# Performance work log

Hardware: AMD Instinct MI355X
Metric: run time of the kernel (lower is better)

Reference implementation:

```python
import jax, jax.numpy as jnp
import numpy as np

N = 200_000   # nodes in batched graph
E = 400_000   # edges
D = 128       # embed_dim
L = 5         # num_layer
G = 1000      # number of graphs in batch
ATOM_V = 119  # atom vocab (OGB)
BOND_V = 5    # bond vocab (OGB)
OUT = 128     # output_dim
EPS = 1e-5


def setup_inputs() -> dict:
    key = jax.random.key(0)
    ks = jax.random.split(key, 16)
    inp = {
        "nfeat": jax.random.randint(ks[0], (N,), 0, ATOM_V),
        "efeat": jax.random.randint(ks[1], (E,), 0, BOND_V),
        "src": jax.random.randint(ks[2], (E,), 0, N),
        "dst": jax.random.randint(ks[3], (E,), 0, N),
        "node2graph": jnp.sort(jax.random.randint(ks[4], (N,), 0, G)),
        # learned parameters
        "atom_emb": jax.random.normal(ks[5], (ATOM_V, D), jnp.float32) * 0.02,
        "edge_emb": jax.random.normal(ks[6], (L, BOND_V, D), jnp.float32) * 0.02,
        "W": jax.random.normal(ks[7], (L, D, D), jnp.float32) * 0.02,
        "b": jnp.zeros((L, D), jnp.float32),
        "gamma": jnp.ones((L, D), jnp.float32),
        "beta": jnp.zeros((L, D), jnp.float32),
        "W1": jax.random.normal(ks[8], (D, D), jnp.float32) * 0.02,
        "b1": jnp.zeros((D,), jnp.float32),
        "W2": jax.random.normal(ks[9], (D, OUT), jnp.float32) * 0.02,
        "b2": jnp.zeros((OUT,), jnp.float32),
    }
    return inp


def reference(nfeat, efeat, src, dst, node2graph,
              atom_emb, edge_emb, W, b, gamma, beta, W1, b1, W2, b2):
    h = atom_emb[nfeat]                                  # [N, D]
    # in-degree + 1 (GCNConvLayer degree norm)
    deg = jax.ops.segment_sum(jnp.ones((E,), h.dtype), dst, num_segments=N) + 1.0
    for l in range(L):
        e = edge_emb[l][efeat]                           # [E, D] edge encoder
        m = h[src] + e                                   # u_add_e
        neigh = jax.ops.segment_sum(m, dst, num_segments=N)  # fn.sum -> 'neigh'
        h = ((h + neigh) / deg[:, None]) @ W[l] + b[l]   # project_node_feat
        # batch norm over nodes (training-mode batch stats), affine
        mu = jnp.mean(h, axis=0)
        var = jnp.var(h, axis=0)
        h = (h - mu) * jax.lax.rsqrt(var + EPS) * gamma[l] + beta[l]
        h = jax.nn.relu(h)                               # activation; dropout=eval
    # global mean pooling per graph
    cnt = jax.ops.segment_sum(jnp.ones((N,), h.dtype), node2graph, num_segments=G)
    g = jax.ops.segment_sum(h, node2graph, num_segments=G) / jnp.maximum(cnt, 1.0)[:, None]
    # predict MLP (dropout in eval mode = identity)
    out = jax.nn.relu(g @ W1 + b1) @ W2 + b2             # [G, OUT]
    return out
```

## Files before the change

kernel.cpp:

```cpp
#include <hip/hip_runtime.h>
#include <hip/hip_bf16.h>
#include <cstddef>

#define NN 200000
#define NE 400000
#define DD 128
#define NL 5
#define NG 1000
#define BOND_V 5
#define BM 32
#define NBLK (NN / BM)
#define MAXD 16
#define PCH 200
#define NB_SCAN 200
#define CH 1000
#define SB 125
#define EPS 1e-5f
#define XS 136

typedef __bf16 bf16x8 __attribute__((ext_vector_type(8)));
typedef float floatx4 __attribute__((ext_vector_type(4)));

__device__ __forceinline__ unsigned short f2bf(float f) {
    unsigned int u = __float_as_uint(f);
    u = (u + 0x7fffu + ((u >> 16) & 1u)) >> 16;
    return (unsigned short)u;
}
__device__ __forceinline__ float bf2f(unsigned short s) {
    return __uint_as_float(((unsigned int)s) << 16);
}
__device__ __forceinline__ float4 bf4_to_f4(uint2 v) {
    float4 o;
    o.x = __uint_as_float(v.x << 16);
    o.y = __uint_as_float(v.x & 0xffff0000u);
    o.z = __uint_as_float(v.y << 16);
    o.w = __uint_as_float(v.y & 0xffff0000u);
    return o;
}
__device__ __forceinline__ float4 actv4(float4 h, float4 sc, float4 sh) {
    float4 o;
    o.x = fmaxf(0.f, h.x * sc.x + sh.x);
    o.y = fmaxf(0.f, h.y * sc.y + sh.y);
    o.z = fmaxf(0.f, h.z * sc.z + sh.z);
    o.w = fmaxf(0.f, h.w * sc.w + sh.w);
    return o;
}

__global__ void k_setup1(const int* __restrict__ dst, int* __restrict__ cnt,
                         const int* __restrict__ n2g, float* __restrict__ gcnt,
                         const float* __restrict__ W, unsigned short* __restrict__ Wht,
                         unsigned short* __restrict__ Wlt) {
    int e = blockIdx.x * blockDim.x + threadIdx.x;
    if (e < NE) atomicAdd(&cnt[dst[e]], 1);
    if (e < NN) atomicAdd(&gcnt[n2g[e]], 1.0f);
    if (e < NL * DD * DD) {
        int l = e / (DD * DD), rem = e % (DD * DD);
        int k = rem / DD, n = rem % DD;
        float v = W[e];
        unsigned short hb = f2bf(v);
        unsigned short lb = f2bf(v - bf2f(hb));
        size_t o = (size_t)l * DD * DD + (size_t)n * DD + k;
        Wht[o] = hb; Wlt[o] = lb;
    }
}

__global__ void k_scan1(const int* __restrict__ cnt, int* __restrict__ bsum) {
    __shared__ int sh[256];
    int b = blockIdx.x, t = threadIdx.x;
    int s = 0;
    if (t < CH / 4) {
        int base = b * CH + t * 4;
        s = cnt[base] + cnt[base + 1] + cnt[base + 2] + cnt[base + 3];
    }
    sh[t] = s;
    __syncthreads();
    if (t == 0) {
        int tot = 0;
        for (int i = 0; i < CH / 4; i++) tot += sh[i];
        bsum[b] = tot;
    }
}

__global__ void k_scan2(const int* __restrict__ bsum, int* __restrict__ bpre,
                        int* __restrict__ off) {
    if (threadIdx.x == 0) {
        int run = 0;
        for (int i = 0; i < NB_SCAN; i++) { bpre[i] = run; run += bsum[i]; }
        off[NN] = NE;
    }
}

__global__ void k_scan3(const int* __restrict__ cnt, const int* __restrict__ bpre,
                        int* __restrict__ off, int* __restrict__ cur,
                        float* __restrict__ rdeg) {
    __shared__ int sh[256];
    int b = blockIdx.x, t = threadIdx.x;
    int base = b * CH + t * 4;
    int c0 = 0, c1 = 0, c2 = 0, c3 = 0, s = 0;
    if (t < CH / 4) {
        c0 = cnt[base]; c1 = cnt[base + 1]; c2 = cnt[base + 2]; c3 = cnt[base + 3];
        s = c0 + c1 + c2 + c3;
    }
    sh[t] = s;
    __syncthreads();
    if (t == 0) {
        int run = bpre[b];
        for (int i = 0; i < CH / 4; i++) { int v = sh[i]; sh[i] = run; run += v; }
    }
    __syncthreads();
    if (t < CH / 4) {
        int run = sh[t];
        off[base] = run; cur[base] = run; run += c0;
        off[base + 1] = run; cur[base + 1] = run; run += c1;
        off[base + 2] = run; cur[base + 2] = run; run += c2;
        off[base + 3] = run; cur[base + 3] = run;
        rdeg[base]     = 1.0f / (float)(c0 + 1);
        rdeg[base + 1] = 1.0f / (float)(c1 + 1);
        rdeg[base + 2] = 1.0f / (float)(c2 + 1);
        rdeg[base + 3] = 1.0f / (float)(c3 + 1);
    }
}

__global__ void k_bucket(const int* __restrict__ src, const int* __restrict__ dst,
                         const int* __restrict__ efeat, int* __restrict__ cur,
                         int* __restrict__ esrc, int* __restrict__ eft) {
    int e = blockIdx.x * blockDim.x + threadIdx.x;
    if (e < NE) {
        int p = atomicAdd(&cur[dst[e]], 1);
        esrc[p] = src[e];
        eft[p] = efeat[e];
    }
}

__global__ void k_pad(const int* __restrict__ off, const int* __restrict__ esrc,
                      const int* __restrict__ eft, const int* __restrict__ nfeat,
                      int* __restrict__ pent, int* __restrict__ pent0,
                      int* __restrict__ bperm, int* __restrict__ gmax) {
    __shared__ int offL[BM + 1];
    __shared__ int degS[BM];
    __shared__ int sortIdx[BM];
    int b = blockIdx.x, tid = threadIdx.x;
    if (tid <= BM) offL[tid] = off[b * BM + tid];
    __syncthreads();
    if (tid < BM) degS[tid] = offL[tid + 1] - offL[tid];
    __syncthreads();
    if (tid < BM) {
        int d = degS[tid], rank = 0;
        #pragma unroll
        for (int j = 0; j < BM; j++)
            rank += (degS[j] > d) || (degS[j] == d && j < tid);
        sortIdx[rank] = tid;
    }
    __syncthreads();
    if (tid < 8) gmax[b * 8 + tid] = degS[sortIdx[tid * 4]];
    if (tid < BM) bperm[b * BM + tid] = sortIdx[tid];
    __syncthreads();
    for (int idx = tid; idx < BM * MAXD; idx += 256) {
        int p = idx & 31, j = idx >> 5;
        int row = sortIdx[p];
        int d = degS[row];
        int v, v0;
        if (j < d) {
            int e = offL[row] + j;
            int s = esrc[e], f = eft[e];
            v = s | (f << 18);
            v0 = nfeat[s] | (f << 18);
        } else { v = (5 << 18); v0 = (5 << 18); }
        pent[(size_t)b * MAXD * BM + j * BM + p] = v;
        pent0[(size_t)b * MAXD * BM + j * BM + p] = v0;
    }
}

__global__ __launch_bounds__(256, 6)
void k_fused(const void* __restrict__ basep, const int* __restrict__ nfeat, int first,
             const int* __restrict__ off, const int* __restrict__ esrc,
             const int* __restrict__ eft, const int* __restrict__ pentsel,
             const int* __restrict__ bperm, const int* __restrict__ gmax,
             const float* __restrict__ eemb, const float* __restrict__ rdeg,
             const float* __restrict__ scP, const float* __restrict__ shP,
             const unsigned short* __restrict__ Wht, const unsigned short* __restrict__ Wlt,
             const float* __restrict__ bias,
             unsigned short* __restrict__ C, float* __restrict__ part) {
    __shared__ unsigned short Xh[BM * XS];
    __shared__ unsigned short Xl[BM * XS];
    __shared__ float eSr[6 * DD];
    __shared__ int pentL[BM * MAXD];

    const float* baseF = (const float*)basep;
    const unsigned short* baseB = (const unsigned short*)basep;

    int tid = threadIdx.x;
    int n0 = blockIdx.x * BM;
    if (tid < 160) *(float4*)(eSr + tid * 4) = *(const float4*)(eemb + tid * 4);
    else if (tid < 192) *(float4*)(eSr + tid * 4) = (float4){0.f, 0.f, 0.f, 0.f};
    {
        const int2* pg = (const int2*)(pentsel + (size_t)blockIdx.x * MAXD * BM);
        *(int2*)(pentL + tid * 2) = pg[tid];
    }

    int lane32 = tid & 31, grp = tid >> 5;
    int c4 = lane32 << 2;
    float4 sc4, sh4;
    if (!first) {
        sc4 = *(const float4*)(scP + c4);
        sh4 = *(const float4*)(shP + c4);
    }

    int rows[4];
    #pragma unroll
    for (int i = 0; i < 4; i++) rows[i] = bperm[blockIdx.x * BM + grp * 4 + i];
    int gmx = gmax[blockIdx.x * 8 + grp];

    float4 acc[4];
    #pragma unroll
    for (int i = 0; i < 4; i++) {
        int n = n0 + rows[i];
        if (first) {
            acc[i] = *(const float4*)(baseF + (size_t)nfeat[n] * DD + c4);
        } else {
            uint2 g = *(const uint2*)(baseB + (size_t)n * DD + c4);
            acc[i] = actv4(bf4_to_f4(g), sc4, sh4);
        }
    }
    __syncthreads();

    int jE = gmx < MAXD ? gmx : MAXD;
    jE = (jE + 1) & ~1;
    const int* pL = pentL + grp * 4;

    if (first) {
        for (int j = 0; j < jE; j += 2) {
            int a0 = pL[j*32+0], a1 = pL[j*32+1], a2 = pL[j*32+2], a3 = pL[j*32+3];
            int b0 = pL[j*32+32], b1 = pL[j*32+33], b2 = pL[j*32+34], b3 = pL[j*32+35];
            float4 ha0 = *(const float4*)(baseF + (size_t)(a0 & 0x3FFFF) * DD + c4);
            float4 ha1 = *(const float4*)(baseF + (size_t)(a1 & 0x3FFFF) * DD + c4);
            float4 ha2 = *(const float4*)(baseF + (size_t)(a2 & 0x3FFFF) * DD + c4);
            float4 ha3 = *(const float4*)(baseF + (size_t)(a3 & 0x3FFFF) * DD + c4);
            float4 hb0 = *(const float4*)(baseF + (size_t)(b0 & 0x3FFFF) * DD + c4);
            float4 hb1 = *(const float4*)(baseF + (size_t)(b1 & 0x3FFFF) * DD + c4);
            float4 hb2 = *(const float4*)(baseF + (size_t)(b2 & 0x3FFFF) * DD + c4);
            float4 hb3 = *(const float4*)(baseF + (size_t)(b3 & 0x3FFFF) * DD + c4);
            int fa0 = a0 >> 18, fa1 = a1 >> 18, fa2 = a2 >> 18, fa3 = a3 >> 18;
            int fb0 = b0 >> 18, fb1 = b1 >> 18, fb2 = b2 >> 18, fb3 = b3 >> 18;
            float wa0 = (fa0 == 5) ? 0.f : 1.f, wa1 = (fa1 == 5) ? 0.f : 1.f;
            float wa2 = (fa2 == 5) ? 0.f : 1.f, wa3 = (fa3 == 5) ? 0.f : 1.f;
            float wb0 = (fb0 == 5) ? 0.f : 1.f, wb1 = (fb1 == 5) ? 0.f : 1.f;
            float wb2 = (fb2 == 5) ? 0.f : 1.f, wb3 = (fb3 == 5) ? 0.f : 1.f;
            float4 ea0 = *(const float4*)(eSr + fa0 * DD + c4);
            float4 ea1 = *(const float4*)(eSr + fa1 * DD + c4);
            float4 ea2 = *(const float4*)(eSr + fa2 * DD + c4);
            float4 ea3 = *(const float4*)(eSr + fa3 * DD + c4);
            float4 eb0 = *(const float4*)(eSr + fb0 * DD + c4);
            float4 eb1 = *(const float4*)(eSr + fb1 * DD + c4);
            float4 eb2 = *(const float4*)(eSr + fb2 * DD + c4);
            float4 eb3 = *(const float4*)(eSr + fb3 * DD + c4);
            acc[0].x += (ha0.x + ea0.x) * wa0 + (hb0.x + eb0.x) * wb0;
            acc[0].y += (ha0.y + ea0.y) * wa0 + (hb0.y + eb0.y) * wb0;
            acc[0].z += (ha0.z + ea0.z) * wa0 + (hb0.z + eb0.z) * wb0;
            acc[0].w += (ha0.w + ea0.w) * wa0 + (hb0.w + eb0.w) * wb0;
            acc[1].x += (ha1.x + ea1.x) * wa1 + (hb1.x + eb1.x) * wb1;
            acc[1].y += (ha1.y + ea1.y) * wa1 + (hb1.y + eb1.y) * wb1;
            acc[1].z += (ha1.z + ea1.z) * wa1 + (hb1.z + eb1.z) * wb1;
            acc[1].w += (ha1.w + ea1.w) * wa1 + (hb1.w + eb1.w) * wb1;
            acc[2].x += (ha2.x + ea2.x) * wa2 + (hb2.x + eb2.x) * wb2;
            acc[2].y += (ha2.y + ea2.y) * wa2 + (hb2.y + eb2.y) * wb2;
            acc[2].z += (ha2.z + ea2.z) * wa2 + (hb2.z + eb2.z) * wb2;
            acc[2].w += (ha2.w + ea2.w) * wa2 + (hb2.w + eb2.w) * wb2;
            acc[3].x += (ha3.x + ea3.x) * wa3 + (hb3.x + eb3.x) * wb3;
            acc[3].y += (ha3.y + ea3.y) * wa3 + (hb3.y + eb3.y) * wb3;
            acc[3].z += (ha3.z + ea3.z) * wa3 + (hb3.z + eb3.z) * wb3;
            acc[3].w += (ha3.w + ea3.w) * wa3 + (hb3.w + eb3.w) * wb3;
        }
    } else {
        int pa0 = pL[0], pa1 = pL[1], pa2 = pL[2], pa3 = pL[3];
        uint2 ga0 = *(const uint2*)(baseB + (size_t)(pa0 & 0x3FFFF) * DD + c4);
        uint2 ga1 = *(const uint2*)(baseB + (size_t)(pa1 & 0x3FFFF) * DD + c4);
        uint2 ga2 = *(const uint2*)(baseB + (size_t)(pa2 & 0x3FFFF) * DD + c4);
        uint2 ga3 = *(const uint2*)(baseB + (size_t)(pa3 & 0x3FFFF) * DD + c4);
        #pragma unroll 1
        for (int j = 0; j < jE; j += 2) {
            int pb0 = pL[(j+1)*32+0], pb1 = pL[(j+1)*32+1];
            int pb2 = pL[(j+1)*32+2], pb3 = pL[(j+1)*32+3];
            uint2 gb0 = *(const uint2*)(baseB + (size_t)(pb0 & 0x3FFFF) * DD + c4);
            uint2 gb1 = *(const uint2*)(baseB + (size_t)(pb1 & 0x3FFFF) * DD + c4);
            uint2 gb2 = *(const uint2*)(baseB + (size_t)(pb2 & 0x3FFFF) * DD + c4);
            uint2 gb3 = *(const uint2*)(baseB + (size_t)(pb3 & 0x3FFFF) * DD + c4);
            {
                float4 h0 = actv4(bf4_to_f4(ga0), sc4, sh4);
                float4 h1 = actv4(bf4_to_f4(ga1), sc4, sh4);
                float4 h2 = actv4(bf4_to_f4(ga2), sc4, sh4);
                float4 h3 = actv4(bf4_to_f4(ga3), sc4, sh4);
                int f0 = pa0 >> 18, f1 = pa1 >> 18, f2 = pa2 >> 18, f3 = pa3 >> 18;
                float w0 = (f0 == 5) ? 0.f : 1.f, w1 = (f1 == 5) ? 0.f : 1.f;
                float w2 = (f2 == 5) ? 0.f : 1.f, w3 = (f3 == 5) ? 0.f : 1.f;
                float4 e0 = *(const float4*)(eSr + f0 * DD + c4);
                float4 e1 = *(const float4*)(eSr + f1 * DD + c4);
                float4 e2 = *(const float4*)(eSr + f2 * DD + c4);
                float4 e3 = *(const float4*)(eSr + f3 * DD + c4);
                acc[0].x += (h0.x + e0.x) * w0; acc[0].y += (h0.y + e0.y) * w0;
                acc[0].z += (h0.z + e0.z) * w0; acc[0].w += (h0.w + e0.w) * w0;
                acc[1].x += (h1.x + e1.x) * w1; acc[1].y += (h1.y + e1.y) * w1;
                acc[1].z += (h1.z + e1.z) * w1; acc[1].w += (h1.w + e1.w) * w1;
                acc[2].x += (h2.x + e2.x) * w2; acc[2].y += (h2.y + e2.y) * w2;
                acc[2].z += (h2.z + e2.z) * w2; acc[2].w += (h2.w + e2.w) * w2;
                acc[3].x += (h3.x + e3.x) * w3; acc[3].y += (h3.y + e3.y) * w3;
                acc[3].z += (h3.z + e3.z) * w3; acc[3].w += (h3.w + e3.w) * w3;
            }
            int j2 = (j + 2 < MAXD) ? (j + 2) : (MAXD - 1);
            pa0 = pL[j2*32+0]; pa1 = pL[j2*32+1]; pa2 = pL[j2*32+2]; pa3 = pL[j2*32+3];
            ga0 = *(const uint2*)(baseB + (size_t)(pa0 & 0x3FFFF) * DD + c4);
            ga1 = *(const uint2*)(baseB + (size_t)(pa1 & 0x3FFFF) * DD + c4);
            ga2 = *(const uint2*)(baseB + (size_t)(pa2 & 0x3FFFF) * DD + c4);
            ga3 = *(const uint2*)(baseB + (size_t)(pa3 & 0x3FFFF) * DD + c4);
            {
                float4 h0 = actv4(bf4_to_f4(gb0), sc4, sh4);
                float4 h1 = actv4(bf4_to_f4(gb1), sc4, sh4);
                float4 h2 = actv4(bf4_to_f4(gb2), sc4, sh4);
                float4 h3 = actv4(bf4_to_f4(gb3), sc4, sh4);
                int f0 = pb0 >> 18, f1 = pb1 >> 18, f2 = pb2 >> 18, f3 = pb3 >> 18;
                float w0 = (f0 == 5) ? 0.f : 1.f, w1 = (f1 == 5) ? 0.f : 1.f;
                float w2 = (f2 == 5) ? 0.f : 1.f, w3 = (f3 == 5) ? 0.f : 1.f;
                float4 e0 = *(const float4*)(eSr + f0 * DD + c4);
                float4 e1 = *(const float4*)(eSr + f1 * DD + c4);
                float4 e2 = *(const float4*)(eSr + f2 * DD + c4);
                float4 e3 = *(const float4*)(eSr + f3 * DD + c4);
                acc[0].x += (h0.x + e0.x) * w0; acc[0].y += (h0.y + e0.y) * w0;
                acc[0].z += (h0.z + e0.z) * w0; acc[0].w += (h0.w + e0.w) * w0;
                acc[1].x += (h1.x + e1.x) * w1; acc[1].y += (h1.y + e1.y) * w1;
                acc[1].z += (h1.z + e1.z) * w1; acc[1].w += (h1.w + e1.w) * w1;
                acc[2].x += (h2.x + e2.x) * w2; acc[2].y += (h2.y + e2.y) * w2;
                acc[2].z += (h2.z + e2.z) * w2; acc[2].w += (h2.w + e2.w) * w2;
                acc[3].x += (h3.x + e3.x) * w3; acc[3].y += (h3.y + e3.y) * w3;
                acc[3].z += (h3.z + e3.z) * w3; acc[3].w += (h3.w + e3.w) * w3;
            }
        }
    }

    if (gmx > MAXD) {
        #pragma unroll
        for (int i = 0; i < 4; i++) {
            int row = rows[i];
            int e0 = off[n0 + row] + MAXD, e1 = off[n0 + row + 1];
            for (int e = e0; e < e1; e++) {
                int s = esrc[e], f = eft[e];
                float4 hv;
                if (first) {
                    hv = *(const float4*)(baseF + (size_t)nfeat[s] * DD + c4);
                } else {
                    uint2 g = *(const uint2*)(baseB + (size_t)s * DD + c4);
                    hv = actv4(bf4_to_f4(g), sc4, sh4);
                }
                const float* ep = eSr + f * DD + c4;
                acc[i].x += hv.x + ep[0]; acc[i].y += hv.y + ep[1];
                acc[i].z += hv.z + ep[2]; acc[i].w += hv.w + ep[3];
            }
        }
    }

    #pragma unroll
    for (int i = 0; i < 4; i++) {
        int r = rows[i];
        float rd = rdeg[n0 + r];
        float ax = acc[i].x * rd, ay = acc[i].y * rd, az = acc[i].z * rd, aw = acc[i].w * rd;
        unsigned short h0 = f2bf(ax), h1 = f2bf(ay), h2 = f2bf(az), h3 = f2bf(aw);
        unsigned short l0 = f2bf(ax - bf2f(h0));
        unsigned short l1 = f2bf(ay - bf2f(h1));
        unsigned short l2 = f2bf(az - bf2f(h2));
        unsigned short l3 = f2bf(aw - bf2f(h3));
        uint2 hv2, lv2;
        hv2.x = (unsigned)h0 | ((unsigned)h1 << 16);
        hv2.y = (unsigned)h2 | ((unsigned)h3 << 16);
        lv2.x = (unsigned)l0 | ((unsigned)l1 << 16);
        lv2.y = (unsigned)l2 | ((unsigned)l3 << 16);
        *(uint2*)(Xh + r * XS + c4) = hv2;
        *(uint2*)(Xl + r * XS + c4) = lv2;
    }
    __syncthreads();

    int lane = tid & 63, w = tid >> 6;
    int m16 = lane & 15, quad = lane >> 4;
    int rowTile = w & 1;
    int colBase = (w >> 1) << 6;
    int rowA = rowTile * 16 + m16;

    floatx4 acc4[4];
    #pragma unroll
    for (int t = 0; t < 4; t++) acc4[t] = (floatx4){0.f, 0.f, 0.f, 0.f};

    #pragma unroll
    for (int kp = 0; kp < 4; kp++) {
        bf16x8 ah = *(const bf16x8*)(Xh + rowA * XS + kp * 32 + quad * 8);
        bf16x8 al = *(const bf16x8*)(Xl + rowA * XS + kp * 32 + quad * 8);
        #pragma unroll
        for (int t = 0; t < 4; t++) {
            int ncol = colBase + t * 16 + m16;
            bf16x8 bh = *(const bf16x8*)(Wht + (size_t)ncol * DD + kp * 32 + quad * 8);
            bf16x8 bl = *(const bf16x8*)(Wlt + (size_t)ncol * DD + kp * 32 + quad * 8);
            acc4[t] = __builtin_amdgcn_mfma_f32_16x16x32_bf16(ah, bh, acc4[t], 0, 0, 0);
            acc4[t] = __builtin_amdgcn_mfma_f32_16x16x32_bf16(ah, bl, acc4[t], 0, 0, 0);
            acc4[t] = __builtin_amdgcn_mfma_f32_16x16x32_bf16(al, bh, acc4[t], 0, 0, 0);
        }
    }
    __syncthreads();

    float* redS = eSr;
    float* redQ = eSr + 2 * DD;
    unsigned short* Cs = Xh;
    #pragma unroll
    for (int t = 0; t < 4; t++) {
        int col = colBase + t * 16 + m16;
        float bv = bias[col];
        float s = 0.f, q = 0.f;
        #pragma unroll
        for (int rr = 0; rr < 4; rr++) {
            float vv = acc4[t][rr] + bv;
            s += vv; q += vv * vv;
            Cs[(rowTile * 16 + quad * 4 + rr) * XS + col] = f2bf(vv);
        }
        s += __shfl_xor(s, 16); q += __shfl_xor(q, 16);
        s += __shfl_xor(s, 32); q += __shfl_xor(q, 32);
        if (lane < 16) { redS[rowTile * DD + col] = s; redQ[rowTile * DD + col] = q; }
    }
    __syncthreads();

    #pragma unroll
    for (int it = 0; it < 2; it++) {
        int idx = it * 256 + tid;
        int row = idx >> 4, q16 = idx & 15;
        uint4 v = *(const uint4*)(Cs + row * XS + q16 * 8);
        *(uint4*)(C + (size_t)(n0 + row) * DD + q16 * 8) = v;
    }
    if (tid < DD) {
        float ss = redS[tid] + redS[DD + tid];
        float qq = redQ[tid] + redQ[DD + tid];
        part[(size_t)blockIdx.x * 256 + tid] = ss;
        part[(size_t)blockIdx.x * 256 + DD + tid] = qq;
    }
}

__global__ void k_stats(const float* __restrict__ part, float* __restrict__ acc,
                        int* __restrict__ cnt,
                        const float* __restrict__ gamma, const float* __restrict__ beta,
                        float* __restrict__ scale, float* __restrict__ shift) {
    int t = threadIdx.x;
    float s = 0.f;
    int base = blockIdx.x * (NBLK / SB);
    for (int i = 0; i < NBLK / SB; i++)
        s += part[(size_t)(base + i) * 256 + t];
    atomicAdd(&acc[t], s);
    __threadfence();
    __shared__ int lastS;
    __syncthreads();
    if (t == 0) lastS = (atomicAdd(cnt, 1) == SB - 1);
    __syncthreads();
    if (lastS && t < DD) {
        float Sv = atomicAdd(&acc[t], 0.0f);
        float Qv = atomicAdd(&acc[DD + t], 0.0f);
        float m = Sv / (float)NN;
        float v = Qv / (float)NN - m * m;
        float rs = rsqrtf(v + EPS);
        float sc = rs * gamma[t];
        scale[t] = sc;
        shift[t] = beta[t] - m * sc;
    }
}

__global__ void k_bnpool(const unsigned short* __restrict__ A, const int* __restrict__ n2g,
                         const float* __restrict__ scale, const float* __restrict__ shift,
                         float* __restrict__ gsum) {
    int tid = threadIdx.x;
    int stripe = tid >> 5, lane = tid & 31;
    int c4 = lane << 2;
    int n0 = blockIdx.x * PCH;
    float4 sc4 = *(const float4*)(scale + c4);
    float4 sh4 = *(const float4*)(shift + c4);
    float4 acc = {0.f, 0.f, 0.f, 0.f};
    int cur = n2g[n0 + stripe];
    for (int i = 0; i < PCH / 8; i++) {
        int n = n0 + i * 8 + stripe;
        int gg = n2g[n];
        if (gg != cur) {
            atomicAdd(&gsum[(size_t)cur * DD + c4 + 0], acc.x);
            atomicAdd(&gsum[(size_t)cur * DD + c4 + 1], acc.y);
            atomicAdd(&gsum[(size_t)cur * DD + c4 + 2], acc.z);
            atomicAdd(&gsum[(size_t)cur * DD + c4 + 3], acc.w);
            acc = (float4){0.f, 0.f, 0.f, 0.f};
            cur = gg;
        }
        uint2 v = *(const uint2*)(A + (size_t)n * DD + c4);
        float4 x = bf4_to_f4(v);
        acc.x += fmaxf(0.f, x.x * sc4.x + sh4.x);
        acc.y += fmaxf(0.f, x.y * sc4.y + sh4.y);
        acc.z += fmaxf(0.f, x.z * sc4.z + sh4.z);
        acc.w += fmaxf(0.f, x.w * sc4.w + sh4.w);
    }
    atomicAdd(&gsum[(size_t)cur * DD + c4 + 0], acc.x);
    atomicAdd(&gsum[(size_t)cur * DD + c4 + 1], acc.y);
    atomicAdd(&gsum[(size_t)cur * DD + c4 + 2], acc.z);
    atomicAdd(&gsum[(size_t)cur * DD + c4 + 3], acc.w);
}

__global__ void k_mlp(const float* __restrict__ gsum, const float* __restrict__ gcnt,
                      const float* __restrict__ W1, const float* __restrict__ b1,
                      const float* __restrict__ W2, const float* __restrict__ b2,
                      float* __restrict__ out) {
    __shared__ float gs[DD], hs[DD];
    int gid = blockIdx.x, j = threadIdx.x;
    float inv = 1.0f / fmaxf(gcnt[gid], 1.0f);
    gs[j] = gsum[(size_t)gid * DD + j] * inv;
    __syncthreads();
    float a = b1[j];
    for (int k = 0; k < DD; k++) a += gs[k] * W1[k * DD + j];
    hs[j] = fmaxf(a, 0.f);
    __syncthreads();
    float o = b2[j];
    for (int k = 0; k < DD; k++) o += hs[k] * W2[k * DD + j];
    out[(size_t)gid * DD + j] = o;
}

extern "C" void kernel_launch(void* const* d_in, const int* in_sizes, int n_in,
                              void* d_out, int out_size, void* d_ws, size_t ws_size,
                              hipStream_t stream) {
    const int*   nfeat = (const int*)d_in[0];
    const int*   efeat = (const int*)d_in[1];
    const int*   src   = (const int*)d_in[2];
    const int*   dst   = (const int*)d_in[3];
    const int*   n2g   = (const int*)d_in[4];
    const float* aemb  = (const float*)d_in[5];
    const float* eemb  = (const float*)d_in[6];
    const float* Wl    = (const float*)d_in[7];
    const float* bl    = (const float*)d_in[8];
    const float* gam   = (const float*)d_in[9];
    const float* bet   = (const float*)d_in[10];
    const float* W1    = (const float*)d_in[11];
    const float* b1    = (const float*)d_in[12];
    const float* W2    = (const float*)d_in[13];
    const float* b2    = (const float*)d_in[14];
    float* out = (float*)d_out;

    unsigned short* H0 = (unsigned short*)d_ws;
    unsigned short* H1 = H0 + (size_t)NN * DD;
    float* rdeg   = (float*)(H1 + (size_t)NN * DD);
    float* gsum   = rdeg + NN;
    float* gcnt   = gsum + (size_t)NG * DD;
    float* scaleA = gcnt + NG;
    float* shiftA = scaleA + NL * DD;
    float* accS   = shiftA + NL * DD;
    int*   scnt   = (int*)(accS + NL * 256);
    float* part   = (float*)(scnt + 16);
    unsigned short* Wht = (unsigned short*)(part + (size_t)NBLK * 256);
    unsigned short* Wlt = Wht + (size_t)NL * DD * DD;
    int* off   = (int*)(Wlt + (size_t)NL * DD * DD);
    int* cur   = off + NN + 1;
    int* esrc  = cur + NN;
    int* eft   = esrc + NE;
    int* cnt   = eft + NE;
    int* bsum  = cnt + NN;
    int* bpre  = bsum + NB_SCAN;
    int* bperm = bpre + NB_SCAN;
    int* gmax  = bperm + (size_t)NBLK * BM;
    int* pent  = gmax + (size_t)NBLK * 8;
    int* pent0 = pent + (size_t)NBLK * MAXD * BM;

    hipMemsetAsync(gsum, 0, (size_t)(NG * DD + NG) * sizeof(float), stream);
    hipMemsetAsync(accS, 0, (size_t)(NL * 256) * sizeof(float) + 16 * sizeof(int), stream);
    hipMemsetAsync(cnt, 0, (size_t)NN * sizeof(int), stream);

    k_setup1<<<(NE + 255) / 256, 256, 0, stream>>>(dst, cnt, n2g, gcnt, Wl, Wht, Wlt);
    k_scan1<<<NB_SCAN, 256, 0, stream>>>(cnt, bsum);
    k_scan2<<<1, 64, 0, stream>>>(bsum, bpre, off);
    k_scan3<<<NB_SCAN, 256, 0, stream>>>(cnt, bpre, off, cur, rdeg);
    k_bucket<<<(NE + 255) / 256, 256, 0, stream>>>(src, dst, efeat, cur, esrc, eft);
    k_pad<<<NBLK, 256, 0, stream>>>(off, esrc, eft, nfeat, pent, pent0, bperm, gmax);

    unsigned short* hcur = H0;
    for (int l = 0; l < NL; l++) {
        const void* base = (l == 0) ? (const void*)aemb : (const void*)hcur;
        unsigned short* hnext = (l == 0) ? H0 : ((hcur == H0) ? H1 : H0);
        const int* psel = (l == 0) ? pent0 : pent;
        const float* scP = scaleA + (size_t)((l == 0) ? 0 : (l - 1)) * DD;
        const float* shP = shiftA + (size_t)((l == 0) ? 0 : (l - 1)) * DD;
        k_fused<<<NBLK, 256, 0, stream>>>(base, nfeat, (l == 0) ? 1 : 0,
                                          off, esrc, eft, psel, bperm, gmax,
                                          eemb + (size_t)l * BOND_V * DD, rdeg,
                                          scP, shP,
                                          Wht + (size_t)l * DD * DD,
                                          Wlt + (size_t)l * DD * DD,
                                          bl + (size_t)l * DD, hnext, part);
        k_stats<<<SB, 256, 0, stream>>>(part, accS + l * 256, scnt + l,
                                        gam + (size_t)l * DD, bet + (size_t)l * DD,
                                        scaleA + (size_t)l * DD, shiftA + (size_t)l * DD);
        hcur = hnext;
    }
    k_bnpool<<<NN / PCH, 256, 0, stream>>>(hcur, n2g,
                                           scaleA + (size_t)(NL - 1) * DD,
                                           shiftA + (size_t)(NL - 1) * DD, gsum);
    k_mlp<<<NG, DD, 0, stream>>>(gsum, gcnt, W1, b1, W2, b2, out);
}
```

Measured before the change: 1.221 ms.

## Replace padded per-row edge tables with edge-parallel CSR aggregation via LDS atomics

Result: slower. 1.862 ms (+52.5%).

```diff
diff --git a/kernel.cpp b/kernel.cpp
--- a/kernel.cpp
+++ b/kernel.cpp
@@ -10,13 +10,13 @@
 #define BOND_V 5
 #define BM 32
 #define NBLK (NN / BM)
-#define MAXD 16
 #define PCH 200
 #define NB_SCAN 200
 #define CH 1000
 #define SB 125
 #define EPS 1e-5f
 #define XS 136
+#define XF 132
 
 typedef __bf16 bf16x8 __attribute__((ext_vector_type(8)));
 typedef float floatx4 __attribute__((ext_vector_type(4)));
@@ -122,258 +122,187 @@
 }
 
 __global__ void k_bucket(const int* __restrict__ src, const int* __restrict__ dst,
-                         const int* __restrict__ efeat, int* __restrict__ cur,
-                         int* __restrict__ esrc, int* __restrict__ eft) {
+                         const int* __restrict__ efeat, const int* __restrict__ nfeat,
+                         int* __restrict__ cur,
+                         int* __restrict__ pe, int* __restrict__ pe0) {
     int e = blockIdx.x * blockDim.x + threadIdx.x;
     if (e < NE) {
-        int p = atomicAdd(&cur[dst[e]], 1);
-        esrc[p] = src[e];
-        eft[p] = efeat[e];
-    }
-}
-
-__global__ void k_pad(const int* __restrict__ off, const int* __restrict__ esrc,
-                      const int* __restrict__ eft, const int* __restrict__ nfeat,
-                      int* __restrict__ pent, int* __restrict__ pent0,
-                      int* __restrict__ bperm, int* __restrict__ gmax) {
-    __shared__ int offL[BM + 1];
-    __shared__ int degS[BM];
-    __shared__ int sortIdx[BM];
-    int b = blockIdx.x, tid = threadIdx.x;
-    if (tid <= BM) offL[tid] = off[b * BM + tid];
-    __syncthreads();
-    if (tid < BM) degS[tid] = offL[tid + 1] - offL[tid];
-    __syncthreads();
-    if (tid < BM) {
-        int d = degS[tid], rank = 0;
-        #pragma unroll
-        for (int j = 0; j < BM; j++)
-            rank += (degS[j] > d) || (degS[j] == d && j < tid);
-        sortIdx[rank] = tid;
-    }
-    __syncthreads();
-    if (tid < 8) gmax[b * 8 + tid] = degS[sortIdx[tid * 4]];
-    if (tid < BM) bperm[b * BM + tid] = sortIdx[tid];
-    __syncthreads();
-    for (int idx = tid; idx < BM * MAXD; idx += 256) {
-        int p = idx & 31, j = idx >> 5;
-        int row = sortIdx[p];
-        int d = degS[row];
-        int v, v0;
-        if (j < d) {
-            int e = offL[row] + j;
-            int s = esrc[e], f = eft[e];
-            v = s | (f << 18);
-            v0 = nfeat[s] | (f << 18);
-        } else { v = (5 << 18); v0 = (5 << 18); }
-        pent[(size_t)b * MAXD * BM + j * BM + p] = v;
-        pent0[(size_t)b * MAXD * BM + j * BM + p] = v0;
-    }
-}
-
-__global__ __launch_bounds__(256, 6)
+        int d = dst[e];
+        int p = atomicAdd(&cur[d], 1);
+        int s = src[e], f = efeat[e], r = d & 31;
+        int hi = (f << 18) | (r << 21);
+        pe[p]  = s | hi;
+        pe0[p] = nfeat[s] | hi;
+    }
+}
+
+__global__ __launch_bounds__(256, 4)
 void k_fused(const void* __restrict__ basep, const int* __restrict__ nfeat, int first,
-             const int* __restrict__ off, const int* __restrict__ esrc,
-             const int* __restrict__ eft, const int* __restrict__ pentsel,
-             const int* __restrict__ bperm, const int* __restrict__ gmax,
+             const int* __restrict__ off, const int* __restrict__ pe,
              const float* __restrict__ eemb, const float* __restrict__ rdeg,
              const float* __restrict__ scP, const float* __restrict__ shP,
              const unsigned short* __restrict__ Wht, const unsigned short* __restrict__ Wlt,
              const float* __restrict__ bias,
              unsigned short* __restrict__ C, float* __restrict__ part) {
-    __shared__ unsigned short Xh[BM * XS];
-    __shared__ unsigned short Xl[BM * XS];
-    __shared__ float eSr[6 * DD];
-    __shared__ int pentL[BM * MAXD];
+    __shared__ __align__(16) unsigned char Ubuf[BM * XS * 2 * 2];
+    __shared__ float eSrF[6 * XF];
+    __shared__ float scS[DD], shS[DD];
+    __shared__ int peL[256];
+
+    float* X = (float*)Ubuf;
+    unsigned short* Xh = (unsigned short*)Ubuf;
+    unsigned short* Xl = Xh + BM * XS;
 
     const float* baseF = (const float*)basep;
     const unsigned short* baseB = (const unsigned short*)basep;
 
     int tid = threadIdx.x;
     int n0 = blockIdx.x * BM;
-    if (tid < 160) *(float4*)(eSr + tid * 4) = *(const float4*)(eemb + tid * 4);
-    else if (tid < 192) *(float4*)(eSr + tid * 4) = (float4){0.f, 0.f, 0.f, 0.f};
+
+    if (tid < 160) {
+        int i = tid * 4; int f = i >> 7, c = i & 127;
+        *(float4*)(eSrF + f * XF + c) = *(const float4*)(eemb + i);
+    } else if (tid < 192) {
+        int c = (tid - 160) * 4;
+        *(float4*)(scS + c) = *(const float4*)(scP + c);
+    } else if (tid < 224) {
+        int c = (tid - 192) * 4;
+        *(float4*)(shS + c) = *(const float4*)(shP + c);
+    }
+    int eBeg = off[n0], eEnd = off[n0 + BM];
+    int nE = eEnd - eBeg;
+    if (tid < nE) peL[tid] = pe[eBeg + tid];
+    __syncthreads();
+
+    int s_slot = tid >> 4, le = tid & 15, d0 = le * 8;
+    int irow = tid >> 3, iseg = tid & 7, idim = iseg * 16;
+
+    float4 scA, scB, shA, shB;
+    if (!first) {
+        scA = *(const float4*)(scS + d0);     scB = *(const float4*)(scS + d0 + 4);
+        shA = *(const float4*)(shS + d0);     shB = *(const float4*)(shS + d0 + 4);
+    }
+
+    int nT = (nE + 15) >> 4;
+
+    int pk0 = 0; bool v0 = (s_slot < nE);
+    if (v0) pk0 = peL[s_slot];
+    uint4 g0u = {0, 0, 0, 0};
+    float4 g0a, g0b;
+    if (first) {
+        if (v0) {
+            const float* hp = baseF + (size_t)(pk0 & 0x3FFFF) * DD + d0;
+            g0a = *(const float4*)hp; g0b = *(const float4*)(hp + 4);
+        }
+    } else {
+        if (v0) g0u = *(const uint4*)(baseB + (size_t)(pk0 & 0x3FFFF) * DD + d0);
+    }
+    float rd = rdeg[n0 + irow];
+
     {
-        const int2* pg = (const int2*)(pentsel + (size_t)blockIdx.x * MAXD * BM);
-        *(int2*)(pentL + tid * 2) = pg[tid];
-    }
-
-    int lane32 = tid & 31, grp = tid >> 5;
-    int c4 = lane32 << 2;
-    float4 sc4, sh4;
-    if (!first) {
-        sc4 = *(const float4*)(scP + c4);
-        sh4 = *(const float4*)(shP + c4);
-    }
-
-    int rows[4];
+        float4 w0, w1, w2, w3;
+        if (first) {
+            int a = nfeat[n0 + irow];
+            const float* ap = baseF + (size_t)a * DD + idim;
+            w0 = *(const float4*)ap;       w1 = *(const float4*)(ap + 4);
+            w2 = *(const float4*)(ap + 8); w3 = *(const float4*)(ap + 12);
+        } else {
+            const unsigned short* hp = baseB + (size_t)(n0 + irow) * DD + idim;
+            uint4 p0 = *(const uint4*)hp, p1 = *(const uint4*)(hp + 8);
+            uint2 u0; u0.x = p0.x; u0.y = p0.y;
+            uint2 u1; u1.x = p0.z; u1.y = p0.w;
+            uint2 u2; u2.x = p1.x; u2.y = p1.y;
+            uint2 u3; u3.x = p1.z; u3.y = p1.w;
+            w0 = actv4(bf4_to_f4(u0), *(const float4*)(scS + idim),      *(const float4*)(shS + idim));
+            w1 = actv4(bf4_to_f4(u1), *(const float4*)(scS + idim + 4),  *(const float4*)(shS + idim + 4));
+            w2 = actv4(bf4_to_f4(u2), *(const float4*)(scS + idim + 8),  *(const float4*)(shS + idim + 8));
+            w3 = actv4(bf4_to_f4(u3), *(const float4*)(scS + idim + 12), *(const float4*)(shS + idim + 12));
+        }
+        float* xp = X + irow * XF + idim;
+        *(float4*)(xp + 0) = w0;  *(float4*)(xp + 4)  = w1;
+        *(float4*)(xp + 8) = w2;  *(float4*)(xp + 12) = w3;
+    }
+    __syncthreads();
+
+    if (first) {
+        int i0 = s_slot;
+        for (int t = 0; t < nT; ++t) {
+            int i1 = i0 + 16;
+            bool v1 = (i1 < nE);
+            int pk1 = 0; float4 g1a = {0,0,0,0}, g1b = {0,0,0,0};
+            if (v1) {
+                pk1 = (i1 < 256) ? peL[i1] : pe[eBeg + i1];
+                const float* hp = baseF + (size_t)(pk1 & 0x3FFFF) * DD + d0;
+                g1a = *(const float4*)hp; g1b = *(const float4*)(hp + 4);
+            }
+            if (v0) {
+                int f = (pk0 >> 18) & 7, row = (pk0 >> 21) & 31;
+                const float* ep = eSrF + f * XF + d0;
+                float4 eA = *(const float4*)ep, eB = *(const float4*)(ep + 4);
+                float* xp = X + row * XF + d0;
+                atomicAdd(xp + 0, g0a.x + eA.x); atomicAdd(xp + 1, g0a.y + eA.y);
+                atomicAdd(xp + 2, g0a.z + eA.z); atomicAdd(xp + 3, g0a.w + eA.w);
+                atomicAdd(xp + 4, g0b.x + eB.x); atomicAdd(xp + 5, g0b.y + eB.y);
+                atomicAdd(xp + 6, g0b.z + eB.z); atomicAdd(xp + 7, g0b.w + eB.w);
+            }
+            pk0 = pk1; g0a = g1a; g0b = g1b; v0 = v1; i0 = i1;
+        }
+    } else {
+        int i0 = s_slot;
+        for (int t = 0; t < nT; ++t) {
+            int i1 = i0 + 16;
+            bool v1 = (i1 < nE);
+            int pk1 = 0; uint4 g1 = {0, 0, 0, 0};
+            if (v1) {
+                pk1 = (i1 < 256) ? peL[i1] : pe[eBeg + i1];
+                g1 = *(const uint4*)(baseB + (size_t)(pk1 & 0x3FFFF) * DD + d0);
+            }
+            if (v0) {
+                int f = (pk0 >> 18) & 7, row = (pk0 >> 21) & 31;
+                uint2 u0; u0.x = g0u.x; u0.y = g0u.y;
+                uint2 u1; u1.x = g0u.z; u1.y = g0u.w;
+                float4 hA = actv4(bf4_to_f4(u0), scA, shA);
+                float4 hB = actv4(bf4_to_f4(u1), scB, shB);
+                const float* ep = eSrF + f * XF + d0;
+                float4 eA = *(const float4*)ep, eB = *(const float4*)(ep + 4);
+                float* xp = X + row * XF + d0;
+                atomicAdd(xp + 0, hA.x + eA.x); atomicAdd(xp + 1, hA.y + eA.y);
+                atomicAdd(xp + 2, hA.z + eA.z); atomicAdd(xp + 3, hA.w + eA.w);
+                atomicAdd(xp + 4, hB.x + eB.x); atomicAdd(xp + 5, hB.y + eB.y);
+                atomicAdd(xp + 6, hB.z + eB.z); atomicAdd(xp + 7, hB.w + eB.w);
+            }
+            pk0 = pk1; g0u = g1; v0 = v1; i0 = i1;
+        }
+    }
+    __syncthreads();
+
+    float rv[16];
+    {
+        const float* xp = X + irow * XF + idim;
+        float4 a0 = *(const float4*)(xp + 0), a1 = *(const float4*)(xp + 4);
+        float4 a2 = *(const float4*)(xp + 8), a3 = *(const float4*)(xp + 12);
+        rv[0]  = a0.x * rd; rv[1]  = a0.y * rd; rv[2]  = a0.z * rd; rv[3]  = a0.w * rd;
+        rv[4]  = a1.x * rd; rv[5]  = a1.y * rd; rv[6]  = a1.z * rd; rv[7]  = a1.w * rd;
+        rv[8]  = a2.x * rd; rv[9]  = a2.y * rd; rv[10] = a2.z * rd; rv[11] = a2.w * rd;
+        rv[12] = a3.x * rd; rv[13] = a3.y * rd; rv[14] = a3.z * rd; rv[15] = a3.w * rd;
+    }
+    __syncthreads();
     #pragma unroll
-    for (int i = 0; i < 4; i++) rows[i] = bperm[blockIdx.x * BM + grp * 4 + i];
-    int gmx = gmax[blockIdx.x * 8 + grp];
-
-    float4 acc[4];
-    #pragma unroll
-    for (int i = 0; i < 4; i++) {
-        int n = n0 + rows[i];
-        if (first) {
-            acc[i] = *(const float4*)(baseF + (size_t)nfeat[n] * DD + c4);
-        } else {
-            uint2 g = *(const uint2*)(baseB + (size_t)n * DD + c4);
-            acc[i] = actv4(bf4_to_f4(g), sc4, sh4);
-        }
-    }
-    __syncthreads();
-
-    int jE = gmx < MAXD ? gmx : MAXD;
-    jE = (jE + 1) & ~1;
-    const int* pL = pentL + grp * 4;
-
-    if (first) {
-        for (int j = 0; j < jE; j += 2) {
-            int a0 = pL[j*32+0], a1 = pL[j*32+1], a2 = pL[j*32+2], a3 = pL[j*32+3];
-            int b0 = pL[j*32+32], b1 = pL[j*32+33], b2 = pL[j*32+34], b3 = pL[j*32+35];
-            float4 ha0 = *(const float4*)(baseF + (size_t)(a0 & 0x3FFFF) * DD + c4);
-            float4 ha1 = *(const float4*)(baseF + (size_t)(a1 & 0x3FFFF) * DD + c4);
-            float4 ha2 = *(const float4*)(baseF + (size_t)(a2 & 0x3FFFF) * DD + c4);
-            float4 ha3 = *(const float4*)(baseF + (size_t)(a3 & 0x3FFFF) * DD + c4);
-            float4 hb0 = *(const float4*)(baseF + (size_t)(b0 & 0x3FFFF) * DD + c4);
-            float4 hb1 = *(const float4*)(baseF + (size_t)(b1 & 0x3FFFF) * DD + c4);
-            float4 hb2 = *(const float4*)(baseF + (size_t)(b2 & 0x3FFFF) * DD + c4);
-            float4 hb3 = *(const float4*)(baseF + (size_t)(b3 & 0x3FFFF) * DD + c4);
-            int fa0 = a0 >> 18, fa1 = a1 >> 18, fa2 = a2 >> 18, fa3 = a3 >> 18;
-            int fb0 = b0 >> 18, fb1 = b1 >> 18, fb2 = b2 >> 18, fb3 = b3 >> 18;
-            float wa0 = (fa0 == 5) ? 0.f : 1.f, wa1 = (fa1 == 5) ? 0.f : 1.f;
-            float wa2 = (fa2 == 5) ? 0.f : 1.f, wa3 = (fa3 == 5) ? 0.f : 1.f;
-            float wb0 = (fb0 == 5) ? 0.f : 1.f, wb1 = (fb1 == 5) ? 0.f : 1.f;
-            float wb2 = (fb2 == 5) ? 0.f : 1.f, wb3 = (fb3 == 5) ? 0.f : 1.f;
-            float4 ea0 = *(const float4*)(eSr + fa0 * DD + c4);
-            float4 ea1 = *(const float4*)(eSr + fa1 * DD + c4);
-            float4 ea2 = *(const float4*)(eSr + fa2 * DD + c4);
-            float4 ea3 = *(const float4*)(eSr + fa3 * DD + c4);
-            float4 eb0 = *(const float4*)(eSr + fb0 * DD + c4);
-            float4 eb1 = *(const float4*)(eSr + fb1 * DD + c4);
-            float4 eb2 = *(const float4*)(eSr + fb2 * DD + c4);
-            float4 eb3 = *(const float4*)(eSr + fb3 * DD + c4);
-            acc[0].x += (ha0.x + ea0.x) * wa0 + (hb0.x + eb0.x) * wb0;
-            acc[0].y += (ha0.y + ea0.y) * wa0 + (hb0.y + eb0.y) * wb0;
-            acc[0].z += (ha0.z + ea0.z) * wa0 + (hb0.z + eb0.z) * wb0;
-            acc[0].w += (ha0.w + ea0.w) * wa0 + (hb0.w + eb0.w) * wb0;
-            acc[1].x += (ha1.x + ea1.x) * wa1 + (hb1.x + eb1.x) * wb1;
-            acc[1].y += (ha1.y + ea1.y) * wa1 + (hb1.y + eb1.y) * wb1;
-            acc[1].z += (ha1.z + ea1.z) * wa1 + (hb1.z + eb1.z) * wb1;
-            acc[1].w += (ha1.w + ea1.w) * wa1 + (hb1.w + eb1.w) * wb1;
-            acc[2].x += (ha2.x + ea2.x) * wa2 + (hb2.x + eb2.x) * wb2;
-            acc[2].y += (ha2.y + ea2.y) * wa2 + (hb2.y + eb2.y) * wb2;
-            acc[2].z += (ha2.z + ea2.z) * wa2 + (hb2.z + eb2.z) * wb2;
-            acc[2].w += (ha2.w + ea2.w) * wa2 + (hb2.w + eb2.w) * wb2;
-            acc[3].x += (ha3.x + ea3.x) * wa3 + (hb3.x + eb3.x) * wb3;
-            acc[3].y += (ha3.y + ea3.y) * wa3 + (hb3.y + eb3.y) * wb3;
-            acc[3].z += (ha3.z + ea3.z) * wa3 + (hb3.z + eb3.z) * wb3;
-            acc[3].w += (ha3.w + ea3.w) * wa3 + (hb3.w + eb3.w) * wb3;
-        }
-    } else {
-        int pa0 = pL[0], pa1 = pL[1], pa2 = pL[2], pa3 = pL[3];
-        uint2 ga0 = *(const uint2*)(baseB + (size_t)(pa0 & 0x3FFFF) * DD + c4);
-        uint2 ga1 = *(const uint2*)(baseB + (size_t)(pa1 & 0x3FFFF) * DD + c4);
-        uint2 ga2 = *(const uint2*)(baseB + (size_t)(pa2 & 0x3FFFF) * DD + c4);
-        uint2 ga3 = *(const uint2*)(baseB + (size_t)(pa3 & 0x3FFFF) * DD + c4);
-        #pragma unroll 1
-        for (int j = 0; j < jE; j += 2) {
-            int pb0 = pL[(j+1)*32+0], pb1 = pL[(j+1)*32+1];
-            int pb2 = pL[(j+1)*32+2], pb3 = pL[(j+1)*32+3];
-            uint2 gb0 = *(const uint2*)(baseB + (size_t)(pb0 & 0x3FFFF) * DD + c4);
-            uint2 gb1 = *(const uint2*)(baseB + (size_t)(pb1 & 0x3FFFF) * DD + c4);
-            uint2 gb2 = *(const uint2*)(baseB + (size_t)(pb2 & 0x3FFFF) * DD + c4);
-            uint2 gb3 = *(const uint2*)(baseB + (size_t)(pb3 & 0x3FFFF) * DD + c4);
-            {
-                float4 h0 = actv4(bf4_to_f4(ga0), sc4, sh4);
-                float4 h1 = actv4(bf4_to_f4(ga1), sc4, sh4);
-                float4 h2 = actv4(bf4_to_f4(ga2), sc4, sh4);
-                float4 h3 = actv4(bf4_to_f4(ga3), sc4, sh4);
-                int f0 = pa0 >> 18, f1 = pa1 >> 18, f2 = pa2 >> 18, f3 = pa3 >> 18;
-                float w0 = (f0 == 5) ? 0.f : 1.f, w1 = (f1 == 5) ? 0.f : 1.f;
-                float w2 = (f2 == 5) ? 0.f : 1.f, w3 = (f3 == 5) ? 0.f : 1.f;
-                float4 e0 = *(const float4*)(eSr + f0 * DD + c4);
-                float4 e1 = *(const float4*)(eSr + f1 * DD + c4);
-                float4 e2 = *(const float4*)(eSr + f2 * DD + c4);
-                float4 e3 = *(const float4*)(eSr + f3 * DD + c4);
-                acc[0].x += (h0.x + e0.x) * w0; acc[0].y += (h0.y + e0.y) * w0;
-                acc[0].z += (h0.z + e0.z) * w0; acc[0].w += (h0.w + e0.w) * w0;
-                acc[1].x += (h1.x + e1.x) * w1; acc[1].y += (h1.y + e1.y) * w1;
-                acc[1].z += (h1.z + e1.z) * w1; acc[1].w += (h1.w + e1.w) * w1;
-                acc[2].x += (h2.x + e2.x) * w2; acc[2].y += (h2.y + e2.y) * w2;
-                acc[2].z += (h2.z + e2.z) * w2; acc[2].w += (h2.w + e2.w) * w2;
-                acc[3].x += (h3.x + e3.x) * w3; acc[3].y += (h3.y + e3.y) * w3;
-                acc[3].z += (h3.z + e3.z) * w3; acc[3].w += (h3.w + e3.w) * w3;
-            }
-            int j2 = (j + 2 < MAXD) ? (j + 2) : (MAXD - 1);
-            pa0 = pL[j2*32+0]; pa1 = pL[j2*32+1]; pa2 = pL[j2*32+2]; pa3 = pL[j2*32+3];
-            ga0 = *(const uint2*)(baseB + (size_t)(pa0 & 0x3FFFF) * DD + c4);
-            ga1 = *(const uint2*)(baseB + (size_t)(pa1 & 0x3FFFF) * DD + c4);
-            ga2 = *(const uint2*)(baseB + (size_t)(pa2 & 0x3FFFF) * DD + c4);
-            ga3 = *(const uint2*)(baseB + (size_t)(pa3 & 0x3FFFF) * DD + c4);
-            {
-                float4 h0 = actv4(bf4_to_f4(gb0), sc4, sh4);
-                float4 h1 = actv4(bf4_to_f4(gb1), sc4, sh4);
-                float4 h2 = actv4(bf4_to_f4(gb2), sc4, sh4);
-                float4 h3 = actv4(bf4_to_f4(gb3), sc4, sh4);
-                int f0 = pb0 >> 18, f1 = pb1 >> 18, f2 = pb2 >> 18, f3 = pb3 >> 18;
-                float w0 = (f0 == 5) ? 0.f : 1.f, w1 = (f1 == 5) ? 0.f : 1.f;
-                float w2 = (f2 == 5) ? 0.f : 1.f, w3 = (f3 == 5) ? 0.f : 1.f;
-                float4 e0 = *(const float4*)(eSr + f0 * DD + c4);
-                float4 e1 = *(const float4*)(eSr + f1 * DD + c4);
-                float4 e2 = *(const float4*)(eSr + f2 * DD + c4);
-                float4 e3 = *(const float4*)(eSr + f3 * DD + c4);
-                acc[0].x += (h0.x + e0.x) * w0; acc[0].y += (h0.y + e0.y) * w0;
-                acc[0].z += (h0.z + e0.z) * w0; acc[0].w += (h0.w + e0.w) * w0;
-                acc[1].x += (h1.x + e1.x) * w1; acc[1].y += (h1.y + e1.y) * w1;
-                acc[1].z += (h1.z + e1.z) * w1; acc[1].w += (h1.w + e1.w) * w1;
-                acc[2].x += (h2.x + e2.x) * w2; acc[2].y += (h2.y + e2.y) * w2;
-                acc[2].z += (h2.z + e2.z) * w2; acc[2].w += (h2.w + e2.w) * w2;
-                acc[3].x += (h3.x + e3.x) * w3; acc[3].y += (h3.y + e3.y) * w3;
-                acc[3].z += (h3.z + e3.z) * w3; acc[3].w += (h3.w + e3.w) * w3;
-            }
-        }
-    }
-
-    if (gmx > MAXD) {
-        #pragma unroll
-        for (int i = 0; i < 4; i++) {
-            int row = rows[i];
-            int e0 = off[n0 + row] + MAXD, e1 = off[n0 + row + 1];
-            for (int e = e0; e < e1; e++) {
-                int s = esrc[e], f = eft[e];
-                float4 hv;
-                if (first) {
-                    hv = *(const float4*)(baseF + (size_t)nfeat[s] * DD + c4);
-                } else {
-                    uint2 g = *(const uint2*)(baseB + (size_t)s * DD + c4);
-                    hv = actv4(bf4_to_f4(g), sc4, sh4);
-                }
-                const float* ep = eSr + f * DD + c4;
-                acc[i].x += hv.x + ep[0]; acc[i].y += hv.y + ep[1];
-                acc[i].z += hv.z + ep[2]; acc[i].w += hv.w + ep[3];
-            }
-        }
-    }
-
-    #pragma unroll
-    for (int i = 0; i < 4; i++) {
-        int r = rows[i];
-        float rd = rdeg[n0 + r];
-        float ax = acc[i].x * rd, ay = acc[i].y * rd, az = acc[i].z * rd, aw = acc[i].w * rd;
-        unsigned short h0 = f2bf(ax), h1 = f2bf(ay), h2 = f2bf(az), h3 = f2bf(aw);
-        unsigned short l0 = f2bf(ax - bf2f(h0));
-        unsigned short l1 = f2bf(ay - bf2f(h1));
-        unsigned short l2 = f2bf(az - bf2f(h2));
-        unsigned short l3 = f2bf(aw - bf2f(h3));
-        uint2 hv2, lv2;
-        hv2.x = (unsigned)h0 | ((unsigned)h1 << 16);
-        hv2.y = (unsigned)h2 | ((unsigned)h3 << 16);
-        lv2.x = (unsigned)l0 | ((unsigned)l1 << 16);
-        lv2.y = (unsigned)l2 | ((unsigned)l3 << 16);
-        *(uint2*)(Xh + r * XS + c4) = hv2;
-        *(uint2*)(Xl + r * XS + c4) = lv2;
+    for (int q = 0; q < 4; ++q) {
+        float x0 = rv[q * 4 + 0], x1 = rv[q * 4 + 1];
+        float x2 = rv[q * 4 + 2], x3 = rv[q * 4 + 3];
+        unsigned short h0 = f2bf(x0), h1 = f2bf(x1), h2 = f2bf(x2), h3 = f2bf(x3);
+        unsigned short l0 = f2bf(x0 - bf2f(h0));
+        unsigned short l1 = f2bf(x1 - bf2f(h1));
+        unsigned short l2 = f2bf(x2 - bf2f(h2));
+        unsigned short l3 = f2bf(x3 - bf2f(h3));
+        uint2 hv, lv;
+        hv.x = (unsigned)h0 | ((unsigned)h1 << 16);
+        hv.y = (unsigned)h2 | ((unsigned)h3 << 16);
+        lv.x = (unsigned)l0 | ((unsigned)l1 << 16);
+        lv.y = (unsigned)l2 | ((unsigned)l3 << 16);
+        *(uint2*)(Xh + irow * XS + idim + q * 4) = hv;
+        *(uint2*)(Xl + irow * XS + idim + q * 4) = lv;
     }
     __syncthreads();
 
@@ -403,8 +332,8 @@
     }
     __syncthreads();
 
-    float* redS = eSr;
-    float* redQ = eSr + 2 * DD;
+    float* redS = eSrF;
+    float* redQ = eSrF + 2 * DD;
     unsigned short* Cs = Xh;
     #pragma unroll
     for (int t = 0; t < 4; t++) {
@@ -552,15 +481,11 @@
     unsigned short* Wlt = Wht + (size_t)NL * DD * DD;
     int* off   = (int*)(Wlt + (size_t)NL * DD * DD);
     int* cur   = off + NN + 1;
-    int* esrc  = cur + NN;
-    int* eft   = esrc + NE;
-    int* cnt   = eft + NE;
+    int* cnt   = cur + NN;
     int* bsum  = cnt + NN;
     int* bpre  = bsum + NB_SCAN;
-    int* bperm = bpre + NB_SCAN;
-    int* gmax  = bperm + (size_t)NBLK * BM;
-    int* pent  = gmax + (size_t)NBLK * 8;
-    int* pent0 = pent + (size_t)NBLK * MAXD * BM;
+    int* pe    = bpre + NB_SCAN;
+    int* pe0   = pe + NE;
 
     hipMemsetAsync(gsum, 0, (size_t)(NG * DD + NG) * sizeof(float), stream);
     hipMemsetAsync(accS, 0, (size_t)(NL * 256) * sizeof(float) + 16 * sizeof(int), stream);
@@ -570,18 +495,17 @@
     k_scan1<<<NB_SCAN, 256, 0, stream>>>(cnt, bsum);
     k_scan2<<<1, 64, 0, stream>>>(bsum, bpre, off);
     k_scan3<<<NB_SCAN, 256, 0, stream>>>(cnt, bpre, off, cur, rdeg);
-    k_bucket<<<(NE + 255) / 256, 256, 0, stream>>>(src, dst, efeat, cur, esrc, eft);
-    k_pad<<<NBLK, 256, 0, stream>>>(off, esrc, eft, nfeat, pent, pent0, bperm, gmax);
+    k_bucket<<<(NE + 255) / 256, 256, 0, stream>>>(src, dst, efeat, nfeat, cur, pe, pe0);
 
     unsigned short* hcur = H0;
     for (int l = 0; l < NL; l++) {
         const void* base = (l == 0) ? (const void*)aemb : (const void*)hcur;
         unsigned short* hnext = (l == 0) ? H0 : ((hcur == H0) ? H1 : H0);
-        const int* psel = (l == 0) ? pent0 : pent;
+        const int* psel = (l == 0) ? pe0 : pe;
         const float* scP = scaleA + (size_t)((l == 0) ? 0 : (l - 1)) * DD;
         const float* shP = shiftA + (size_t)((l == 0) ? 0 : (l - 1)) * DD;
         k_fused<<<NBLK, 256, 0, stream>>>(base, nfeat, (l == 0) ? 1 : 0,
-                                          off, esrc, eft, psel, bperm, gmax,
+                                          off, psel,
                                           eemb + (size_t)l * BOND_V * DD, rdeg,
                                           scP, shP,
                                           Wht + (size_t)l * DD * DD,
```
